# Performance work log

Measured on AMD Instinct MI355X. Metric: run time of the kernel, lower is better.

The kernel has to match this reference:

```python
import jax, jax.numpy as jnp
import numpy as np

EMB = 1024
HEADS = 16


def setup_inputs() -> dict:
    key = jax.random.key(0)
    ks = jax.random.split(key, 5)
    s = 1.0 / np.sqrt(EMB).astype(np.float32)
    return {
        "x": jax.random.normal(ks[0], (4, 2048, EMB), dtype=jnp.float32),
        "Wq": jax.random.normal(ks[1], (EMB, EMB), dtype=jnp.float32) * s,
        "bq": jnp.zeros((EMB,), dtype=jnp.float32),
        "Wk": jax.random.normal(ks[2], (EMB, EMB), dtype=jnp.float32) * s,
        "bk": jnp.zeros((EMB,), dtype=jnp.float32),
        "Wv": jax.random.normal(ks[3], (EMB, EMB), dtype=jnp.float32) * s,
        "bv": jnp.zeros((EMB,), dtype=jnp.float32),
        "Wo": jax.random.normal(ks[4], (EMB, EMB), dtype=jnp.float32) * s,
        "bo": jnp.zeros((EMB,), dtype=jnp.float32),
    }


def reference(x, Wq, bq, Wk, bk, Wv, bv, Wo, bo):
    b, n, e = x.shape
    h = HEADS
    d = e // h
    # QKV projections, split heads: [b, n, e] -> [b, h, n, d]
    def split_heads(t):
        return t.reshape(b, n, h, d).transpose(0, 2, 1, 3)
    q = split_heads(x @ Wq + bq)
    k = split_heads(x @ Wk + bk)
    v = split_heads(x @ Wv + bv)
    # NOTE: original scales by sqrt(emb_size), not sqrt(head_dim)
    energy = jnp.einsum('bhqd,bhkd->bhqk', q, k)
    att = jax.nn.softmax(energy / jnp.sqrt(jnp.float32(e)), axis=-1)
    # dropout is identity in eval mode
    out = jnp.einsum('bhqk,bhkd->bhqd', att, v)
    out = out.transpose(0, 2, 1, 3).reshape(b, n, e)
    return out @ Wo + bo
```

## Files before the change

kernel.cpp:

```cpp
#include <hip/hip_runtime.h>

#define EMB   1024
#define SEQ   2048
#define BATCH 4
#define HEADS 16
#define HDIM  64
#define MTOT  8192

typedef __bf16 bf16x8 __attribute__((ext_vector_type(8)));
typedef float  fx4    __attribute__((ext_vector_type(4)));

#if __has_builtin(__builtin_amdgcn_exp2f)
#define EXP2(x) __builtin_amdgcn_exp2f(x)
#else
#define EXP2(x) exp2f(x)
#endif

__device__ __forceinline__ unsigned short f2bf(float f) {
    unsigned u = __builtin_bit_cast(unsigned, f);
    u += 0x7fffu + ((u >> 16) & 1u);
    return (unsigned short)(u >> 16);
}
__device__ __forceinline__ unsigned short bfbits(float f) {
    __bf16 h = (__bf16)f;
    return __builtin_bit_cast(unsigned short, h);
}

#define AS1 __attribute__((address_space(1)))
#define AS3 __attribute__((address_space(3)))
__device__ __forceinline__ void glds16(const void* g, void* l) {
    __builtin_amdgcn_global_load_lds((AS1 void*)g, (AS3 void*)l, 16, 0, 0);
}
#define DRAIN_GLDS() __builtin_amdgcn_s_waitcnt(0x0f70)

#define BAR()    asm volatile("s_barrier" ::: "memory")
#define WAITV8() asm volatile("s_waitcnt vmcnt(8)" ::: "memory")
#define WAITV0() asm volatile("s_waitcnt vmcnt(0)" ::: "memory")

#define QSCALE 0.0450842137604569f

__global__ __launch_bounds__(256) void cvt_x_kernel(const float* __restrict__ x,
                                                    unsigned short* __restrict__ xb)
{
    const int idx = (blockIdx.x * 256 + threadIdx.x) * 4;
    const float4 v = *(const float4*)(x + idx);
    ushort4 o;
    o.x = f2bf(v.x); o.y = f2bf(v.y); o.z = f2bf(v.z); o.w = f2bf(v.w);
    *(ushort4*)(xb + idx) = o;
}

__global__ __launch_bounds__(256) void cvt_w_kernel(
    const float* __restrict__ w0, const float* __restrict__ w1,
    const float* __restrict__ w2, const float* __restrict__ w3,
    unsigned short* __restrict__ o0, unsigned short* __restrict__ o1,
    unsigned short* __restrict__ o2, unsigned short* __restrict__ o3)
{
    const int z = blockIdx.z;
    const float* W = z == 0 ? w0 : (z == 1 ? w1 : (z == 2 ? w2 : w3));
    unsigned short* O = z == 0 ? o0 : (z == 1 ? o1 : (z == 2 ? o2 : o3));

    __shared__ float Ws[64][65];
    const int t  = threadIdx.x;
    const int k0 = blockIdx.x * 64, n0 = blockIdx.y * 64;
#pragma unroll
    for (int p = 0; p < 4; ++p) {
        const int row = p * 16 + (t >> 4);
        const int col = (t & 15) * 4;
        const float4 v = *(const float4*)(W + (size_t)(k0 + row) * EMB + n0 + col);
        Ws[row][col]     = v.x; Ws[row][col + 1] = v.y;
        Ws[row][col + 2] = v.z; Ws[row][col + 3] = v.w;
    }
    __syncthreads();
    const int nn = t >> 2;
    const int kb = (t & 3) * 16;
#pragma unroll
    for (int q = 0; q < 2; ++q) {
        const int kk = kb + q * 8;
        ushort4 u0, u1;
        u0.x = f2bf(Ws[kk + 0][nn]); u0.y = f2bf(Ws[kk + 1][nn]);
        u0.z = f2bf(Ws[kk + 2][nn]); u0.w = f2bf(Ws[kk + 3][nn]);
        u1.x = f2bf(Ws[kk + 4][nn]); u1.y = f2bf(Ws[kk + 5][nn]);
        u1.z = f2bf(Ws[kk + 6][nn]); u1.w = f2bf(Ws[kk + 7][nn]);
        *(ushort4*)(O + (size_t)(n0 + nn) * EMB + k0 + kk)     = u0;
        *(ushort4*)(O + (size_t)(n0 + nn) * EMB + k0 + kk + 4) = u1;
    }
}

__device__ __forceinline__ void stage8(const unsigned short* xp, unsigned short* xd,
                                       const unsigned short* wp, unsigned short* wd)
{
    glds16(xp,            xd);
    glds16(xp +  8 * EMB, xd + 8 * 64);
    glds16(xp + 16 * EMB, xd + 16 * 64);
    glds16(xp + 24 * EMB, xd + 24 * 64);
    glds16(wp,            wd);
    glds16(wp +  8 * EMB, wd + 8 * 64);
    glds16(wp + 16 * EMB, wd + 16 * 64);
    glds16(wp + 24 * EMB, wd + 24 * 64);
}

__global__ __launch_bounds__(512, 2) void gemm_qkv256_kernel(
    const unsigned short* __restrict__ Xg, const unsigned short* __restrict__ Wg,
    const float* __restrict__ bq, const float* __restrict__ bk,
    const float* __restrict__ bv,
    unsigned short* __restrict__ qb, unsigned short* __restrict__ kb,
    unsigned short* __restrict__ vtb)
{
    __shared__ unsigned short Xs[2][256][64];
    __shared__ unsigned short Ws[2][256][64];

    int lin = blockIdx.x;
    lin = (lin & 7) * 48 + (lin >> 3);
    const int bx  = lin & 31;
    const int by  = lin >> 5;
    const int m0  = bx * 256;
    const int e0g = by * 256;

    const int t    = threadIdx.x;
    const int w    = t >> 6;
    const int lane = t & 63;
    const int low4 = lane & 15;
    const int quad = lane >> 4;
    const int wm   = w >> 2;
    const int wn   = w & 3;

    const int r8 = lane >> 3;
    const int sc = (lane & 7) ^ r8;

    const unsigned short* xrow = Xg + (size_t)(m0 + w * 32 + r8) * EMB + sc * 8;
    const unsigned short* wrow = Wg + (size_t)(e0g + w * 32 + r8) * EMB + sc * 8;

    fx4 acc[4][8] = {};

    stage8(xrow,      &Xs[0][w * 32][0], wrow,      &Ws[0][w * 32][0]);
    stage8(xrow + 64, &Xs[1][w * 32][0], wrow + 64, &Ws[1][w * 32][0]);
    WAITV8();
    BAR();

#pragma unroll 2
    for (int kt = 0; kt < 16; ++kt) {
        unsigned short (*Xb)[64] = Xs[kt & 1];
        unsigned short (*Wb)[64] = Ws[kt & 1];

        {
            bf16x8 wf[4], xf[8];
#pragma unroll
            for (int ni = 0; ni < 4; ++ni) {
                const int row = wn * 64 + ni * 16 + low4;
                wf[ni] = *(const bf16x8*)&Wb[row][((quad) ^ (row & 7)) * 8];
            }
#pragma unroll
            for (int mi = 0; mi < 8; ++mi) {
                const int row = wm * 128 + mi * 16 + low4;
                xf[mi] = *(const bf16x8*)&Xb[row][((quad) ^ (row & 7)) * 8];
            }
            BAR();
            __builtin_amdgcn_s_setprio(1);
#pragma unroll
            for (int ni = 0; ni < 4; ++ni)
#pragma unroll
                for (int mi = 0; mi < 8; ++mi)
                    acc[ni][mi] = __builtin_amdgcn_mfma_f32_16x16x32_bf16(
                        wf[ni], xf[mi], acc[ni][mi], 0, 0, 0);
            __builtin_amdgcn_s_setprio(0);
            BAR();
        }
        {
            bf16x8 wf[4], xf[8];
#pragma unroll
            for (int ni = 0; ni < 4; ++ni) {
                const int row = wn * 64 + ni * 16 + low4;
                wf[ni] = *(const bf16x8*)&Wb[row][((4 + quad) ^ (row & 7)) * 8];
            }
#pragma unroll
            for (int mi = 0; mi < 8; ++mi) {
                const int row = wm * 128 + mi * 16 + low4;
                xf[mi] = *(const bf16x8*)&Xb[row][((4 + quad) ^ (row & 7)) * 8];
            }
            BAR();
            __builtin_amdgcn_s_setprio(1);
#pragma unroll
            for (int ni = 0; ni < 4; ++ni)
#pragma unroll
                for (int mi = 0; mi < 8; ++mi)
                    acc[ni][mi] = __builtin_amdgcn_mfma_f32_16x16x32_bf16(
                        wf[ni], xf[mi], acc[ni][mi], 0, 0, 0);
            __builtin_amdgcn_s_setprio(0);
            BAR();
        }
        if (kt + 2 < 16) {
            stage8(xrow + (kt + 2) * 64, &Xb[w * 32][0],
                   wrow + (kt + 2) * 64, &Wb[w * 32][0]);
            WAITV8();
            BAR();
        } else if (kt + 1 < 16) {
            WAITV0();
            BAR();
        }
    }

    const int z   = by >> 2;
    const int eLb = (by & 3) * 256 + wn * 64;
    const float* bias = z == 0 ? bq : (z == 1 ? bk : bv);
    fx4 bvv[4];
#pragma unroll
    for (int ni = 0; ni < 4; ++ni)
        bvv[ni] = *(const fx4*)(bias + eLb + ni * 16 + quad * 4);

    if (z <= 1) {
        const float scl = (z == 0) ? QSCALE : 1.0f;
        unsigned short* o = (z == 0) ? qb : kb;
#pragma unroll
        for (int ni = 0; ni < 4; ++ni)
#pragma unroll
            for (int mi = 0; mi < 8; ++mi) {
                const int m  = m0 + wm * 128 + mi * 16 + low4;
                const int eL = eLb + ni * 16 + quad * 4;
                const int bb = m >> 11, n = m & (SEQ - 1);
                const int hh = eL >> 6, db = eL & 63;
                ushort4 o4;
                o4.x = f2bf((acc[ni][mi][0] + bvv[ni][0]) * scl);
                o4.y = f2bf((acc[ni][mi][1] + bvv[ni][1]) * scl);
                o4.z = f2bf((acc[ni][mi][2] + bvv[ni][2]) * scl);
                o4.w = f2bf((acc[ni][mi][3] + bvv[ni][3]) * scl);
                *(ushort4*)(o + (((size_t)(bb * HEADS + hh)) * SEQ + n) * HDIM + db) = o4;
            }
    } else {
        unsigned short* o = vtb;
#pragma unroll
        for (int ni = 0; ni < 4; ++ni) {
            const int eL = eLb + ni * 16 + quad * 4;
            const int hh = eL >> 6, db = eL & 63;
#pragma unroll
            for (int g = 0; g < 2; ++g) {
                const int mb = m0 + wm * 128 + g * 64;
                const int bb = mb >> 11;
                const int nb = mb & (SEQ - 1);
#pragma unroll
                for (int rr = 0; rr < 4; ++rr) {
                    ushort4 o4;
                    o4.x = f2bf(acc[ni][g * 4 + 0][rr] + bvv[ni][rr]);
                    o4.y = f2bf(acc[ni][g * 4 + 1][rr] + bvv[ni][rr]);
                    o4.z = f2bf(acc[ni][g * 4 + 2][rr] + bvv[ni][rr]);
                    o4.w = f2bf(acc[ni][g * 4 + 3][rr] + bvv[ni][rr]);
                    *(ushort4*)(o + (((size_t)(bb * HEADS + hh)) * HDIM + db + rr) * SEQ
                                  + nb + low4 * 4) = o4;
                }
            }
        }
    }
}

__global__ __launch_bounds__(256) void gemm_bf16_kernel(
    const unsigned short* __restrict__ Ag,
    const unsigned short* __restrict__ B0, const unsigned short* __restrict__ B1,
    const unsigned short* __restrict__ B2,
    const float* __restrict__ bias0, const float* __restrict__ bias1,
    const float* __restrict__ bias2,
    void* out0, void* out1, void* out2, int mode)
{
    const int z = blockIdx.z;
    const unsigned short* __restrict__ Bg = z == 0 ? B0 : (z == 1 ? B1 : B2);
    const float* __restrict__ bias = z == 0 ? bias0 : (z == 1 ? bias1 : bias2);
    void* outp = z == 0 ? out0 : (z == 1 ? out1 : out2);

    __shared__ unsigned short As[128][32];
    __shared__ unsigned short Bs[128][32];

    const int t    = threadIdx.x;
    const int w    = t >> 6;
    const int lane = t & 63;
    const int low4 = lane & 15;
    const int quad = lane >> 4;
    const int m0 = blockIdx.x * 128;
    const int e0 = blockIdx.y * 128;
    const int we = (w & 1) * 64;
    const int wm = (w >> 1) * 64;

    const int srow   = w * 32 + (lane >> 2);
    const int schunk = (lane & 3) ^ ((lane >> 3) & 3);
    const int scol   = schunk * 8;
    const int fchunk = (quad ^ ((low4 >> 1) & 3)) * 8;

    fx4 acc[4][4] = {};

    for (int k0 = 0; k0 < EMB; k0 += 32) {
        __syncthreads();
        glds16(Ag + (size_t)(m0 + srow) * EMB + k0 + scol,      &As[w * 32][0]);
        glds16(Ag + (size_t)(m0 + srow + 16) * EMB + k0 + scol, &As[w * 32 + 16][0]);
        glds16(Bg + (size_t)(e0 + srow) * EMB + k0 + scol,      &Bs[w * 32][0]);
        glds16(Bg + (size_t)(e0 + srow + 16) * EMB + k0 + scol, &Bs[w * 32 + 16][0]);
        DRAIN_GLDS();
        __syncthreads();

        bf16x8 af[4], bfr[4];
#pragma unroll
        for (int i = 0; i < 4; ++i) {
            af[i]  = *(const bf16x8*)&Bs[we + i * 16 + low4][fchunk];
            bfr[i] = *(const bf16x8*)&As[wm + i * 16 + low4][fchunk];
        }
#pragma unroll
        for (int i = 0; i < 4; ++i)
#pragma unroll
            for (int j = 0; j < 4; ++j)
                acc[i][j] = __builtin_amdgcn_mfma_f32_16x16x32_bf16(af[i], bfr[j], acc[i][j], 0, 0, 0);
    }

    fx4 bv[4];
#pragma unroll
    for (int i = 0; i < 4; ++i)
        bv[i] = *(const fx4*)(bias + e0 + we + i * 16 + quad * 4);

    if (mode == 1) {
#pragma unroll
        for (int i = 0; i < 4; ++i)
#pragma unroll
            for (int j = 0; j < 4; ++j) {
                const int m  = m0 + wm + j * 16 + low4;
                const int eb = e0 + we + i * 16 + quad * 4;
                fx4 o4;
#pragma unroll
                for (int rr = 0; rr < 4; ++rr) o4[rr] = acc[i][j][rr] + bv[i][rr];
                *(fx4*)((float*)outp + (size_t)m * EMB + eb) = o4;
            }
    } else if (z <= 1) {
        const float sc = (z == 0) ? QSCALE : 1.0f;
        unsigned short* o = (unsigned short*)outp;
#pragma unroll
        for (int i = 0; i < 4; ++i)
#pragma unroll
            for (int j = 0; j < 4; ++j) {
                const int m  = m0 + wm + j * 16 + low4;
                const int eb = e0 + we + i * 16 + quad * 4;
                const int bb = m >> 11, n = m & (SEQ - 1);
                const int hh = eb >> 6, db = eb & 63;
                ushort4 o4;
                o4.x = f2bf((acc[i][j][0] + bv[i][0]) * sc);
                o4.y = f2bf((acc[i][j][1] + bv[i][1]) * sc);
                o4.z = f2bf((acc[i][j][2] + bv[i][2]) * sc);
                o4.w = f2bf((acc[i][j][3] + bv[i][3]) * sc);
                *(ushort4*)(o + (((size_t)(bb * HEADS + hh)) * SEQ + n) * HDIM + db) = o4;
            }
    } else {
        unsigned short* o = (unsigned short*)outp;
        const int mbase = m0 + wm;
        const int bb    = mbase >> 11;
        const int nb    = mbase & (SEQ - 1);
#pragma unroll
        for (int i = 0; i < 4; ++i) {
            const int eb = e0 + we + i * 16 + quad * 4;
            const int hh = eb >> 6, db = eb & 63;
#pragma unroll
            for (int rr = 0; rr < 4; ++rr) {
                ushort4 o4;
                o4.x = f2bf(acc[i][0][rr] + bv[i][rr]);
                o4.y = f2bf(acc[i][1][rr] + bv[i][rr]);
                o4.z = f2bf(acc[i][2][rr] + bv[i][rr]);
                o4.w = f2bf(acc[i][3][rr] + bv[i][rr]);
                *(ushort4*)(o + (((size_t)(bb * HEADS + hh)) * HDIM + db + rr) * SEQ
                              + nb + low4 * 4) = o4;
            }
        }
    }
}

__global__ __launch_bounds__(256, 2) void attn_mfma5_kernel(
    const unsigned short* __restrict__ qg, const unsigned short* __restrict__ kg,
    const unsigned short* __restrict__ vg, unsigned short* __restrict__ attb)
{
    __shared__ unsigned short Ks[2][64][64];
    __shared__ unsigned short Vs[2][64][64];

    const int t    = threadIdx.x;
    const int w    = t >> 6;
    const int lane = t & 63;
    const int low4 = lane & 15;
    const int quad = lane >> 4;
    const int q0   = blockIdx.x * 256 + w * 64;
    const int bh   = blockIdx.y;
    const size_t base = (size_t)bh * SEQ * HDIM;

    const int srow8  = lane >> 3;
    const int schunk = (lane & 7) ^ srow8;

    const int tr  = 2 * (low4 >> 2) + (low4 & 1) + 8 * ((low4 >> 1) & 1);
    const int x7k = tr & 7;
    const int x7v = low4 & 7;

    bf16x8 aq[4][2];
#pragma unroll
    for (int s = 0; s < 4; ++s) {
        const size_t qrow = base + (size_t)(q0 + s * 16 + low4) * HDIM;
        aq[s][0] = *(const bf16x8*)(qg + qrow + quad * 8);
        aq[s][1] = *(const bf16x8*)(qg + qrow + 32 + quad * 8);
    }

    fx4 o_acc[4][4] = {};
    float l_part[4] = {};
    const fx4 fzero = {0.f, 0.f, 0.f, 0.f};

    {
        const unsigned short* kp = kg + base + (size_t)(w * 16 + srow8) * HDIM + schunk * 8;
        glds16(kp,              &Ks[0][w * 16][0]);
        glds16(kp + 8 * HDIM,   &Ks[0][w * 16 + 8][0]);
        const unsigned short* vp = vg + base + (size_t)(w * 16 + srow8) * SEQ + schunk * 8;
        glds16(vp,              &Vs[0][w * 16][0]);
        glds16(vp + 8 * SEQ,    &Vs[0][w * 16 + 8][0]);
    }

    for (int tt0 = 0; tt0 < SEQ / 64; ++tt0) {
        const int buf = tt0 & 1;
        DRAIN_GLDS();
        __syncthreads();

        bf16x8 kf[4][2], vf[4][2];
#pragma unroll
        for (int tk = 0; tk < 4; ++tk) {
#pragma unroll
            for (int c = 0; c < 2; ++c) {
                kf[tk][c] = *(const bf16x8*)&Ks[buf][tk * 16 + tr][(((c * 4 + quad) ^ x7k)) * 8];
                vf[tk][c] = *(const bf16x8*)&Vs[buf][tk * 16 + low4][(((c * 4 + quad) ^ x7v)) * 8];
            }
        }

        if (tt0 + 1 < SEQ / 64) {
            const int kv1 = (tt0 + 1) * 64;
            const unsigned short* kp = kg + base + (size_t)(kv1 + w * 16 + srow8) * HDIM + schunk * 8;
            glds16(kp,            &Ks[buf ^ 1][w * 16][0]);
            glds16(kp + 8 * HDIM, &Ks[buf ^ 1][w * 16 + 8][0]);
            const unsigned short* vp = vg + base + (size_t)(w * 16 + srow8) * SEQ + kv1 + schunk * 8;
            glds16(vp,            &Vs[buf ^ 1][w * 16][0]);
            glds16(vp + 8 * SEQ,  &Vs[buf ^ 1][w * 16 + 8][0]);
        }

#pragma unroll
        for (int s = 0; s < 4; ++s) {
            fx4 sa[4];
#pragma unroll
            for (int tk = 0; tk < 4; ++tk) {
                sa[tk] = __builtin_amdgcn_mfma_f32_16x16x32_bf16(kf[tk][0], aq[s][0], fzero, 0, 0, 0);
                sa[tk] = __builtin_amdgcn_mfma_f32_16x16x32_bf16(kf[tk][1], aq[s][1], sa[tk], 0, 0, 0);
            }
            float p[4][4];
#pragma unroll
            for (int tk = 0; tk < 4; ++tk)
#pragma unroll
                for (int r = 0; r < 4; ++r)
                    p[tk][r] = EXP2(sa[tk][r]);

            l_part[s] += (((p[0][0] + p[0][1]) + (p[0][2] + p[0][3]))
                        + ((p[1][0] + p[1][1]) + (p[1][2] + p[1][3])))
                       + (((p[2][0] + p[2][1]) + (p[2][2] + p[2][3]))
                        + ((p[3][0] + p[3][1]) + (p[3][2] + p[3][3])));

            bf16x8 pf0, pf1;
#pragma unroll
            for (int tk = 0; tk < 4; ++tk) {
                pf0[tk]     = (__bf16)p[tk][0];
                pf0[4 + tk] = (__bf16)p[tk][1];
                pf1[tk]     = (__bf16)p[tk][2];
                pf1[4 + tk] = (__bf16)p[tk][3];
            }
#pragma unroll
            for (int t2 = 0; t2 < 4; ++t2) {
                o_acc[s][t2] = __builtin_amdgcn_mfma_f32_16x16x32_bf16(vf[t2][0], pf0, o_acc[s][t2], 0, 0, 0);
                o_acc[s][t2] = __builtin_amdgcn_mfma_f32_16x16x32_bf16(vf[t2][1], pf1, o_acc[s][t2], 0, 0, 0);
            }
        }
    }

    float linv[4];
#pragma unroll
    for (int s = 0; s < 4; ++s) {
        float v = l_part[s];
        v += __shfl_xor(v, 16);
        v += __shfl_xor(v, 32);
        linv[s] = 1.0f / v;
    }

    const int bb = bh >> 4, hh = bh & 15;
#pragma unroll
    for (int s = 0; s < 4; ++s) {
        const size_t m = (size_t)bb * SEQ + q0 + s * 16 + low4;
#pragma unroll
        for (int t2 = 0; t2 < 4; ++t2) {
            ushort4 o4;
            o4.x = bfbits(o_acc[s][t2][0] * linv[s]);
            o4.y = bfbits(o_acc[s][t2][1] * linv[s]);
            o4.z = bfbits(o_acc[s][t2][2] * linv[s]);
            o4.w = bfbits(o_acc[s][t2][3] * linv[s]);
            *(ushort4*)(attb + m * EMB + hh * HDIM + t2 * 16 + quad * 4) = o4;
        }
    }
}

extern "C" void kernel_launch(void* const* d_in, const int* in_sizes, int n_in,
                              void* d_out, int out_size, void* d_ws, size_t ws_size,
                              hipStream_t stream)
{
    const float* x  = (const float*)d_in[0];
    const float* Wq = (const float*)d_in[1];
    const float* bq = (const float*)d_in[2];
    const float* Wk = (const float*)d_in[3];
    const float* bk = (const float*)d_in[4];
    const float* Wv = (const float*)d_in[5];
    const float* bv = (const float*)d_in[6];
    const float* Wo = (const float*)d_in[7];
    const float* bo = (const float*)d_in[8];

    unsigned short* ws  = (unsigned short*)d_ws;
    unsigned short* xb  = ws;
    unsigned short* wqt = xb + 8388608;
    unsigned short* wkt = wqt + 1048576;
    unsigned short* wvt = wkt + 1048576;
    unsigned short* wot = wvt + 1048576;
    unsigned short* qb  = wot + 1048576;
    unsigned short* kbuf = qb + 8388608;
    unsigned short* vtb  = kbuf + 8388608;
    unsigned short* attb = vtb + 8388608;

    cvt_x_kernel<<<8192, 256, 0, stream>>>(x, xb);
    cvt_w_kernel<<<dim3(16, 16, 4), 256, 0, stream>>>(Wq, Wk, Wv, Wo, wqt, wkt, wvt, wot);

    gemm_qkv256_kernel<<<384, 512, 0, stream>>>(xb, wqt, bq, bk, bv, qb, kbuf, vtb);

    attn_mfma5_kernel<<<dim3(8, 64), 256, 0, stream>>>(qb, kbuf, vtb, attb);

    gemm_bf16_kernel<<<dim3(64, 8, 1), 256, 0, stream>>>(
        attb, wot, wot, wot, bo, bo, bo, d_out, d_out, d_out, 1);
}
```

Baseline: 287.6 us.

## Restructure QKV GEMM into 4-stage K pipeline and widen output GEMM K-tile

The QKV projection GEMM switches from a double-buffered 64-wide K loop to a 4-slot ring of 32-wide K stages. Each stage issues its global-to-LDS loads split across the two MFMA halves, with a new interleaved row/chunk swizzle and vmcnt-based waits, so memory latency overlaps more compute. Separately, the output projection GEMM doubles its K tile from 32 to 64, halving the number of loop iterations and barriers. This comes at the cost of more LDS use and a more fragile wait-count schedule.

```diff
diff --git a/kernel.cpp b/kernel.cpp
--- a/kernel.cpp
+++ b/kernel.cpp
@@ -35,6 +35,7 @@
 
 #define BAR()    asm volatile("s_barrier" ::: "memory")
 #define WAITV8() asm volatile("s_waitcnt vmcnt(8)" ::: "memory")
+#define WAITV4() asm volatile("s_waitcnt vmcnt(4)" ::: "memory")
 #define WAITV0() asm volatile("s_waitcnt vmcnt(0)" ::: "memory")
 
 #define QSCALE 0.0450842137604569f
@@ -86,28 +87,14 @@
     }
 }
 
-__device__ __forceinline__ void stage8(const unsigned short* xp, unsigned short* xd,
-                                       const unsigned short* wp, unsigned short* wd)
-{
-    glds16(xp,            xd);
-    glds16(xp +  8 * EMB, xd + 8 * 64);
-    glds16(xp + 16 * EMB, xd + 16 * 64);
-    glds16(xp + 24 * EMB, xd + 24 * 64);
-    glds16(wp,            wd);
-    glds16(wp +  8 * EMB, wd + 8 * 64);
-    glds16(wp + 16 * EMB, wd + 16 * 64);
-    glds16(wp + 24 * EMB, wd + 24 * 64);
-}
-
-__global__ __launch_bounds__(512, 2) void gemm_qkv256_kernel(
+__global__ __launch_bounds__(512, 2) void gemm_qkv8p_kernel(
     const unsigned short* __restrict__ Xg, const unsigned short* __restrict__ Wg,
     const float* __restrict__ bq, const float* __restrict__ bk,
     const float* __restrict__ bv,
     unsigned short* __restrict__ qb, unsigned short* __restrict__ kb,
     unsigned short* __restrict__ vtb)
 {
-    __shared__ unsigned short Xs[2][256][64];
-    __shared__ unsigned short Ws[2][256][64];
+    __shared__ unsigned short Ls[4][2][128][64];
 
     int lin = blockIdx.x;
     lin = (lin & 7) * 48 + (lin >> 3);
@@ -124,79 +111,82 @@
     const int wm   = w >> 2;
     const int wn   = w & 3;
 
-    const int r8 = lane >> 3;
-    const int sc = (lane & 7) ^ r8;
-
-    const unsigned short* xrow = Xg + (size_t)(m0 + w * 32 + r8) * EMB + sc * 8;
-    const unsigned short* wrow = Wg + (size_t)(e0g + w * 32 + r8) * EMB + sc * 8;
+    const int mat = w >> 2;
+    const int wr  = w & 3;
+    const int lrl = lane >> 3;
+    const int cch = lane & 7;
+    const int org = cch ^ lrl;
+    const int grow0 = (mat ? e0g : m0) + wr * 64 + 2 * lrl + (org >> 2);
+    const unsigned short* gsrc =
+        (mat ? Wg : Xg) + (size_t)grow0 * EMB + (org & 3) * 8;
+
+    const int l2  = low4 >> 1;
+    const int cs8 = (((((low4 & 1) << 2) | quad)) ^ l2) * 8;
 
     fx4 acc[4][8] = {};
 
-    stage8(xrow,      &Xs[0][w * 32][0], wrow,      &Ws[0][w * 32][0]);
-    stage8(xrow + 64, &Xs[1][w * 32][0], wrow + 64, &Ws[1][w * 32][0]);
+#pragma unroll
+    for (int j = 0; j < 3; ++j) {
+        const unsigned short* gp = gsrc + j * 32;
+        glds16(gp,            &Ls[j][mat][wr * 32 +  0][0]);
+        glds16(gp + 16 * EMB, &Ls[j][mat][wr * 32 +  8][0]);
+        glds16(gp + 32 * EMB, &Ls[j][mat][wr * 32 + 16][0]);
+        glds16(gp + 48 * EMB, &Ls[j][mat][wr * 32 + 24][0]);
+    }
     WAITV8();
     BAR();
 
-#pragma unroll 2
-    for (int kt = 0; kt < 16; ++kt) {
-        unsigned short (*Xb)[64] = Xs[kt & 1];
-        unsigned short (*Wb)[64] = Ws[kt & 1];
-
-        {
-            bf16x8 wf[4], xf[8];
-#pragma unroll
-            for (int ni = 0; ni < 4; ++ni) {
-                const int row = wn * 64 + ni * 16 + low4;
-                wf[ni] = *(const bf16x8*)&Wb[row][((quad) ^ (row & 7)) * 8];
-            }
-#pragma unroll
-            for (int mi = 0; mi < 8; ++mi) {
-                const int row = wm * 128 + mi * 16 + low4;
-                xf[mi] = *(const bf16x8*)&Xb[row][((quad) ^ (row & 7)) * 8];
-            }
-            BAR();
-            __builtin_amdgcn_s_setprio(1);
-#pragma unroll
-            for (int ni = 0; ni < 4; ++ni)
-#pragma unroll
-                for (int mi = 0; mi < 8; ++mi)
-                    acc[ni][mi] = __builtin_amdgcn_mfma_f32_16x16x32_bf16(
-                        wf[ni], xf[mi], acc[ni][mi], 0, 0, 0);
-            __builtin_amdgcn_s_setprio(0);
-            BAR();
-        }
-        {
-            bf16x8 wf[4], xf[8];
-#pragma unroll
-            for (int ni = 0; ni < 4; ++ni) {
-                const int row = wn * 64 + ni * 16 + low4;
-                wf[ni] = *(const bf16x8*)&Wb[row][((4 + quad) ^ (row & 7)) * 8];
-            }
-#pragma unroll
-            for (int mi = 0; mi < 8; ++mi) {
-                const int row = wm * 128 + mi * 16 + low4;
-                xf[mi] = *(const bf16x8*)&Xb[row][((4 + quad) ^ (row & 7)) * 8];
-            }
-            BAR();
-            __builtin_amdgcn_s_setprio(1);
-#pragma unroll
-            for (int ni = 0; ni < 4; ++ni)
-#pragma unroll
-                for (int mi = 0; mi < 8; ++mi)
-                    acc[ni][mi] = __builtin_amdgcn_mfma_f32_16x16x32_bf16(
-                        wf[ni], xf[mi], acc[ni][mi], 0, 0, 0);
-            __builtin_amdgcn_s_setprio(0);
-            BAR();
-        }
-        if (kt + 2 < 16) {
-            stage8(xrow + (kt + 2) * 64, &Xb[w * 32][0],
-                   wrow + (kt + 2) * 64, &Wb[w * 32][0]);
-            WAITV8();
-            BAR();
-        } else if (kt + 1 < 16) {
-            WAITV0();
-            BAR();
-        }
+    for (int s = 0; s < 32; ++s) {
+        const int slot  = s & 3;
+        const int slotd = (s + 3) & 3;
+        const bool st   = (s + 3 < 32);
+        const unsigned short* gp = gsrc + (s + 3) * 32;
+        unsigned short (*LX)[64] = Ls[slot][0];
+        unsigned short (*LW)[64] = Ls[slot][1];
+
+        bf16x8 af[4], xf[4];
+#pragma unroll
+        for (int ni = 0; ni < 4; ++ni)
+            af[ni] = *(const bf16x8*)&LW[wn * 32 + ni * 8 + l2][cs8];
+#pragma unroll
+        for (int j = 0; j < 4; ++j)
+            xf[j] = *(const bf16x8*)&LX[wm * 64 + j * 8 + l2][cs8];
+        if (st) {
+            glds16(gp,            &Ls[slotd][mat][wr * 32 + 0][0]);
+            glds16(gp + 16 * EMB, &Ls[slotd][mat][wr * 32 + 8][0]);
+        }
+        BAR();
+        __builtin_amdgcn_s_setprio(1);
+#pragma unroll
+        for (int ni = 0; ni < 4; ++ni)
+#pragma unroll
+            for (int j = 0; j < 4; ++j)
+                acc[ni][j] = __builtin_amdgcn_mfma_f32_16x16x32_bf16(
+                    af[ni], xf[j], acc[ni][j], 0, 0, 0);
+        __builtin_amdgcn_s_setprio(0);
+        BAR();
+
+        bf16x8 xg[4];
+#pragma unroll
+        for (int j = 0; j < 4; ++j)
+            xg[j] = *(const bf16x8*)&LX[wm * 64 + 32 + j * 8 + l2][cs8];
+        if (st) {
+            glds16(gp + 32 * EMB, &Ls[slotd][mat][wr * 32 + 16][0]);
+            glds16(gp + 48 * EMB, &Ls[slotd][mat][wr * 32 + 24][0]);
+        }
+        if (s < 29)       WAITV8();
+        else if (s == 29) WAITV4();
+        else              WAITV0();
+        BAR();
+        __builtin_amdgcn_s_setprio(1);
+#pragma unroll
+        for (int ni = 0; ni < 4; ++ni)
+#pragma unroll
+            for (int j = 0; j < 4; ++j)
+                acc[ni][4 + j] = __builtin_amdgcn_mfma_f32_16x16x32_bf16(
+                    af[ni], xg[j], acc[ni][4 + j], 0, 0, 0);
+        __builtin_amdgcn_s_setprio(0);
+        BAR();
     }
 
     const int z   = by >> 2;
@@ -264,8 +254,8 @@
     const float* __restrict__ bias = z == 0 ? bias0 : (z == 1 ? bias1 : bias2);
     void* outp = z == 0 ? out0 : (z == 1 ? out1 : out2);
 
-    __shared__ unsigned short As[128][32];
-    __shared__ unsigned short Bs[128][32];
+    __shared__ unsigned short As[128][64];
+    __shared__ unsigned short Bs[128][64];
 
     const int t    = threadIdx.x;
     const int w    = t >> 6;
@@ -277,33 +267,42 @@
     const int we = (w & 1) * 64;
     const int wm = (w >> 1) * 64;
 
-    const int srow   = w * 32 + (lane >> 2);
-    const int schunk = (lane & 3) ^ ((lane >> 3) & 3);
-    const int scol   = schunk * 8;
-    const int fchunk = (quad ^ ((low4 >> 1) & 3)) * 8;
+    const int srow8  = lane >> 3;
+    const int schunk = (lane & 7) ^ srow8;
 
     fx4 acc[4][4] = {};
 
-    for (int k0 = 0; k0 < EMB; k0 += 32) {
+    for (int k0 = 0; k0 < EMB; k0 += 64) {
         __syncthreads();
-        glds16(Ag + (size_t)(m0 + srow) * EMB + k0 + scol,      &As[w * 32][0]);
-        glds16(Ag + (size_t)(m0 + srow + 16) * EMB + k0 + scol, &As[w * 32 + 16][0]);
-        glds16(Bg + (size_t)(e0 + srow) * EMB + k0 + scol,      &Bs[w * 32][0]);
-        glds16(Bg + (size_t)(e0 + srow + 16) * EMB + k0 + scol, &Bs[w * 32 + 16][0]);
+        const unsigned short* ap = Ag + (size_t)(m0 + w * 32 + srow8) * EMB + k0 + schunk * 8;
+        const unsigned short* bp = Bg + (size_t)(e0 + w * 32 + srow8) * EMB + k0 + schunk * 8;
+        glds16(ap,            &As[w * 32 +  0][0]);
+        glds16(ap +  8 * EMB, &As[w * 32 +  8][0]);
+        glds16(ap + 16 * EMB, &As[w * 32 + 16][0]);
+        glds16(ap + 24 * EMB, &As[w * 32 + 24][0]);
+        glds16(bp,            &Bs[w * 32 +  0][0]);
+        glds16(bp +  8 * EMB, &Bs[w * 32 +  8][0]);
+        glds16(bp + 16 * EMB, &Bs[w * 32 + 16][0]);
+        glds16(bp + 24 * EMB, &Bs[w * 32 + 24][0]);
         DRAIN_GLDS();
         __syncthreads();
 
-        bf16x8 af[4], bfr[4];
-#pragma unroll
-        for (int i = 0; i < 4; ++i) {
-            af[i]  = *(const bf16x8*)&Bs[we + i * 16 + low4][fchunk];
-            bfr[i] = *(const bf16x8*)&As[wm + i * 16 + low4][fchunk];
-        }
-#pragma unroll
-        for (int i = 0; i < 4; ++i)
+#pragma unroll
+        for (int ks = 0; ks < 2; ++ks) {
+            const int fch = ((ks * 4 + quad) ^ (low4 & 7)) * 8;
+            bf16x8 af[4], bfr[4];
+#pragma unroll
+            for (int i = 0; i < 4; ++i)
+                af[i] = *(const bf16x8*)&Bs[we + i * 16 + low4][fch];
 #pragma unroll
             for (int j = 0; j < 4; ++j)
-                acc[i][j] = __builtin_amdgcn_mfma_f32_16x16x32_bf16(af[i], bfr[j], acc[i][j], 0, 0, 0);
+                bfr[j] = *(const bf16x8*)&As[wm + j * 16 + low4][fch];
+#pragma unroll
+            for (int i = 0; i < 4; ++i)
+#pragma unroll
+                for (int j = 0; j < 4; ++j)
+                    acc[i][j] = __builtin_amdgcn_mfma_f32_16x16x32_bf16(af[i], bfr[j], acc[i][j], 0, 0, 0);
+        }
     }
 
     fx4 bv[4];
@@ -522,7 +521,7 @@
     cvt_x_kernel<<<8192, 256, 0, stream>>>(x, xb);
     cvt_w_kernel<<<dim3(16, 16, 4), 256, 0, stream>>>(Wq, Wk, Wv, Wo, wqt, wkt, wvt, wot);
 
-    gemm_qkv256_kernel<<<384, 512, 0, stream>>>(xb, wqt, bq, bk, bv, qb, kbuf, vtb);
+    gemm_qkv8p_kernel<<<384, 512, 0, stream>>>(xb, wqt, bq, bk, bv, qb, kbuf, vtb);
 
     attn_mfma5_kernel<<<dim3(8, 64), 256, 0, stream>>>(qb, kbuf, vtb, attb);
 
```

New measurement: 275.6 us. 4.2% less time.
